# Performance work log

Measured on AMD Instinct MI355X. Metric: run time of the kernel, lower is better.

Reference implementation:

```python
import jax, jax.numpy as jnp
import numpy as np

# ---- static config (mirrors init_kwargs) ----
B, N, C_IN, C_OUT = 4, 8192, 128, 256
RATIO = 0.25
M = int(N * RATIO)          # sampled centers per cloud (fps ratio)
RADIUS = 0.1
MAX_NN = 64                 # max_num_neighbors
K = 16                      # num kernel points
D_MID = C_IN // 2           # pre_mlp: in_features -> in_features // 2
KP_EXTENT = RADIUS          # kernel-point influence extent (linear influence)


def setup_inputs() -> dict:
    key = jax.random.key(0)
    ks = jax.random.split(key, 10)
    x = jax.random.normal(ks[0], (B, N, C_IN), jnp.float32)
    pos = jax.random.uniform(ks[1], (B, N, 3), jnp.float32)  # unit cube
    W_pre = jax.random.normal(ks[2], (C_IN, D_MID), jnp.float32) / np.sqrt(C_IN).astype(np.float32)
    b_pre = jnp.zeros((D_MID,), jnp.float32)
    kp_pos = jax.random.normal(ks[3], (K, 3), jnp.float32) * (0.3 * RADIUS)
    kp_W = jax.random.normal(ks[4], (K, D_MID, D_MID), jnp.float32) / np.sqrt(D_MID * K).astype(np.float32)
    W_post = jax.random.normal(ks[5], (D_MID, C_OUT), jnp.float32) / np.sqrt(D_MID).astype(np.float32)
    b_post = jnp.zeros((C_OUT,), jnp.float32)
    W_sc = jax.random.normal(ks[6], (C_IN, C_OUT), jnp.float32) / np.sqrt(C_IN).astype(np.float32)
    b_sc = jnp.zeros((C_OUT,), jnp.float32)
    return dict(x=x, pos=pos, W_pre=W_pre, b_pre=b_pre, kp_pos=kp_pos, kp_W=kp_W,
                W_post=W_post, b_post=b_post, W_sc=W_sc, b_sc=b_sc)


def _fps(p):
    """Farthest point sampling on one cloud p:[N,3] -> idx:[M] (start at point 0)."""
    mind = jnp.sum((p - p[0]) ** 2, axis=-1)  # [N]
    def step(mind, _):
        i = jnp.argmax(mind).astype(jnp.int32)
        mind = jnp.minimum(mind, jnp.sum((p - p[i]) ** 2, axis=-1))
        return mind, i
    _, rest = jax.lax.scan(step, mind, None, length=M - 1)
    return jnp.concatenate([jnp.zeros((1,), jnp.int32), rest])


def reference(x, pos, W_pre, b_pre, kp_pos, kp_W, W_post, b_post, W_sc, b_sc):
    def _cloud(xb, pb):
        # xb:[N,C_IN], pb:[N,3]
        idx = _fps(pb)                                   # [M]
        centers = pb[idx]                                # [M,3]
        # radius neighbor search: nearest MAX_NN, mask to ball of RADIUS
        d2 = jnp.sum((centers[:, None, :] - pb[None, :, :]) ** 2, axis=-1)   # [M,N]
        neg_d2, nn_idx = jax.lax.top_k(-d2, MAX_NN)      # [M,MAX_NN]
        valid = (-neg_d2) <= RADIUS ** 2                 # [M,MAX_NN]
        # pre mlp then gather neighbor features (x_j)
        x_pre = xb @ W_pre + b_pre                       # [N,D_MID]
        x_j = x_pre[nn_idx]                              # [M,MAX_NN,D_MID]
        # kernel-point conv: linear influence of each kernel point
        rel = pb[nn_idx] - centers[:, None, :]           # [M,MAX_NN,3]
        dist = jnp.sqrt(jnp.sum((rel[:, :, None, :] - kp_pos[None, None, :, :]) ** 2, axis=-1) + 1e-12)  # [M,MAX_NN,K]
        infl = jnp.maximum(1.0 - dist / KP_EXTENT, 0.0) * valid[:, :, None]
        # aggregate (sum over neighbors) per kernel point, then contract with kernel weights
        s = jnp.einsum('mek,med->mkd', infl, x_j)        # [M,K,D_MID]
        feat = jnp.einsum('mkd,kdo->mo', s, kp_W)        # [M,D_MID]
        feat = feat @ W_post + b_post                    # [M,C_OUT]
        short = xb[idx] @ W_sc + b_sc                    # residual shortcut on sampled points
        return feat + short, centers

    out_feat, out_pos = jax.vmap(_cloud)(x, pos)         # [B,M,C_OUT], [B,M,3]
    return out_feat, out_pos
```

## Files before the change

### kernel.cpp

```cpp
#include <hip/hip_runtime.h>

#define B_    4
#define N_    8192
#define CIN   128
#define COUT  256
#define M_    2048
#define K_    16
#define DM    64
#define MAXNN 64
#define CAP   128
#define R2    0.01f
#define EXT   0.1f

#define NPRE  1024
#define CONV0 (4 + NPRE)
#define PUB   32

#define FLG(i) ((i) * 32)
#define PREFLG 128

typedef float v2f __attribute__((ext_vector_type(2)));
typedef unsigned long long ull;

__device__ __forceinline__ float d2_exact(float ax, float ay, float az,
                                          float bx, float by, float bz) {
    float dx = ax - bx, dy = ay - by, dz = az - bz;
    return __fadd_rn(__fadd_rn(__fmul_rn(dx, dx), __fmul_rn(dy, dy)), __fmul_rn(dz, dz));
}

#define DPP_STEP2(CTRL)                                                                   \
    {                                                                                     \
        unsigned tlo = (unsigned)__builtin_amdgcn_update_dpp(0, (int)klo, CTRL, 0xF, 0xF, true); \
        unsigned thi = (unsigned)__builtin_amdgcn_update_dpp(0, (int)khi, CTRL, 0xF, 0xF, true); \
        unsigned long long tk = ((unsigned long long)thi << 32) | tlo;                    \
        unsigned long long ck = ((unsigned long long)khi << 32) | klo;                    \
        if (tk > ck) { klo = tlo; khi = thi; }                                            \
    }

__global__ void init_kernel(int* __restrict__ flags) {
    if (threadIdx.x < 160) flags[threadIdx.x] = 0;
}

__global__ __launch_bounds__(512, 2) void mega_kernel(const float* __restrict__ pos,
                                                      int* __restrict__ idx_out,
                                                      float* __restrict__ out_pos,
                                                      const float* __restrict__ x,
                                                      const float* __restrict__ Wp,
                                                      const float* __restrict__ bvec,
                                                      float* __restrict__ xpre,
                                                      const float* __restrict__ kp_pos,
                                                      const float* __restrict__ kp_W,
                                                      const float* __restrict__ W_post,
                                                      const float* __restrict__ b_post,
                                                      const float* __restrict__ W_sc,
                                                      const float* __restrict__ b_sc,
                                                      float* __restrict__ out_feat,
                                                      int* __restrict__ flags) {
    __shared__ union {
        struct { float sx[N_]; float sy[N_]; float sz[N_]; ull slots[2][8]; } f;
        struct { float Ws[CIN * DM]; float xs[32][CIN]; } p;
        struct { int nIdx[CAP]; float nD2[CAP]; int cntS;
                 float infl[MAXNN][K_]; float xj[MAXNN][DM];
                 float sS[K_ * DM]; float featP[4][DM]; float xg[CIN]; } c;
    } sh;

    const int t = threadIdx.x;
    const int blk = blockIdx.x;

    if (blk >= CONV0) {
        const int cid = blk - CONV0;
        const int cb = cid & 3;
        const int cm = cid >> 2;

        if (t == 0) {
            for (;;) {
                int cur = __hip_atomic_load(&flags[FLG(cb)], __ATOMIC_RELAXED, __HIP_MEMORY_SCOPE_AGENT);
                int pre = __hip_atomic_load(&flags[PREFLG], __ATOMIC_RELAXED, __HIP_MEMORY_SCOPE_AGENT);
                if (cur > cm && pre >= NPRE) break;
                int dist = cm - cur;
                if (dist > 512)      __builtin_amdgcn_s_sleep(127);
                else if (dist > 64)  __builtin_amdgcn_s_sleep(32);
                else                 __builtin_amdgcn_s_sleep(8);
            }
            __threadfence();
            sh.c.cntS = 0;
        }
        __syncthreads();

        const float* pb = pos + (size_t)cb * N_ * 3;
        const int ctr = idx_out[cb * M_ + cm];
        const float ccx = pb[ctr * 3 + 0], ccy = pb[ctr * 3 + 1], ccz = pb[ctr * 3 + 2];

        for (int j = 0; j < N_ / 512; j++) {
            int n = j * 512 + t;
            float x0 = pb[n * 3 + 0], y0 = pb[n * 3 + 1], z0 = pb[n * 3 + 2];
            float d = d2_exact(x0, y0, z0, ccx, ccy, ccz);
            if (d <= R2) {
                int pp = atomicAdd(&sh.c.cntS, 1);
                if (pp < CAP) { sh.c.nIdx[pp] = n; sh.c.nD2[pp] = d; }
            }
        }
        __syncthreads();
        int cnt = sh.c.cntS; if (cnt > CAP) cnt = CAP;
        if (cnt > MAXNN) {
            if (t == 0) {
                for (int s = 0; s < MAXNN; s++) {
                    int best = s;
                    for (int q = s + 1; q < cnt; q++) {
                        if (sh.c.nD2[q] < sh.c.nD2[best] ||
                            (sh.c.nD2[q] == sh.c.nD2[best] && sh.c.nIdx[q] < sh.c.nIdx[best])) best = q;
                    }
                    float td = sh.c.nD2[best]; sh.c.nD2[best] = sh.c.nD2[s]; sh.c.nD2[s] = td;
                    int ti = sh.c.nIdx[best]; sh.c.nIdx[best] = sh.c.nIdx[s]; sh.c.nIdx[s] = ti;
                }
            }
            __syncthreads();
            cnt = MAXNN;
        }

        if (t < cnt) {
            int n = sh.c.nIdx[t];
            float rx = pb[n * 3 + 0] - ccx, ry = pb[n * 3 + 1] - ccy, rz = pb[n * 3 + 2] - ccz;
#pragma unroll
            for (int k = 0; k < K_; k++) {
                float dx = rx - kp_pos[k * 3 + 0];
                float dy = ry - kp_pos[k * 3 + 1];
                float dz = rz - kp_pos[k * 3 + 2];
                float dist = sqrtf(dx * dx + dy * dy + dz * dz + 1e-12f);
                sh.c.infl[t][k] = fmaxf(1.0f - dist / EXT, 0.0f);
            }
        }
        for (int i = t; i < cnt * DM; i += 512) {
            int e = i >> 6, d = i & 63;
            sh.c.xj[e][d] = xpre[((size_t)cb * N_ + sh.c.nIdx[e]) * DM + d];
        }
        __syncthreads();

        if (t < 256) {
#pragma unroll
            for (int p4 = 0; p4 < 4; p4++) {
                int pair = t + p4 * 256;
                int k = pair >> 6, d = pair & 63;
                float acc = 0.f;
                for (int e = 0; e < cnt; e++) acc = fmaf(sh.c.infl[e][k], sh.c.xj[e][d], acc);
                sh.c.sS[pair] = acc;
            }
        }
        __syncthreads();

        if (t < 256) {
            int dprime = t & 63, ks = t >> 6;
            float acc = 0.f;
            for (int k = ks * 4; k < ks * 4 + 4; k++) {
                const float* kw = kp_W + ((size_t)k * DM) * DM + dprime;
#pragma unroll
                for (int d = 0; d < DM; d++) acc = fmaf(sh.c.sS[k * DM + d], kw[d * DM], acc);
            }
            sh.c.featP[ks][dprime] = acc;
        }
        __syncthreads();
        if (t < DM) sh.c.featP[0][t] = sh.c.featP[0][t] + sh.c.featP[1][t] + sh.c.featP[2][t] + sh.c.featP[3][t];
        if (t < CIN) sh.c.xg[t] = x[((size_t)cb * N_ + ctr) * CIN + t];
        __syncthreads();

        if (t < 256) {
            const int o = t;
            float acc = b_post[o] + b_sc[o];
#pragma unroll 8
            for (int d = 0; d < DM; d++) acc = fmaf(sh.c.featP[0][d], W_post[d * COUT + o], acc);
#pragma unroll 8
            for (int cc = 0; cc < CIN; cc++) acc = fmaf(sh.c.xg[cc], W_sc[cc * COUT + o], acc);
            out_feat[((size_t)(cb * M_ + cm)) * COUT + o] = acc;
        }
        return;
    }

    if (blk >= 4) {
        const size_t rowBase = (size_t)(blk - 4) * 32;
        for (int i = t; i < CIN * DM; i += 512) sh.p.Ws[i] = Wp[i];
        for (int i = t; i < 32 * CIN; i += 512) {
            int r = i >> 7, c = i & 127;
            sh.p.xs[r][c] = x[(rowBase + r) * CIN + c];
        }
        __syncthreads();
        const int col = t & 63, r0 = t >> 6;
        float acc[4];
        float bias = bvec[col];
#pragma unroll
        for (int rr = 0; rr < 4; rr++) acc[rr] = bias;
        for (int c = 0; c < CIN; c++) {
            float w = sh.p.Ws[c * DM + col];
#pragma unroll
            for (int rr = 0; rr < 4; rr++) acc[rr] = fmaf(sh.p.xs[r0 + 8 * rr][c], w, acc[rr]);
        }
#pragma unroll
        for (int rr = 0; rr < 4; rr++) xpre[(rowBase + r0 + 8 * rr) * DM + col] = acc[rr];
        __threadfence();
        __syncthreads();
        if (t == 0) atomicAdd(&flags[PREFLG], 1);
        return;
    }

    const int b = blk;
    const float* pb = pos + (size_t)b * N_ * 3;

    v2f px[8], py[8], pz[8], mind[8];
#pragma unroll
    for (int jj = 0; jj < 8; jj++) {
        int n0 = t + (2 * jj) * 512, n1 = n0 + 512;
        float x0 = pb[n0 * 3 + 0], y0 = pb[n0 * 3 + 1], z0 = pb[n0 * 3 + 2];
        float x1 = pb[n1 * 3 + 0], y1 = pb[n1 * 3 + 1], z1 = pb[n1 * 3 + 2];
        px[jj] = (v2f){x0, x1};
        py[jj] = (v2f){y0, y1};
        pz[jj] = (v2f){z0, z1};
        mind[jj] = (v2f){1e30f, 1e30f};
        sh.f.sx[n0] = x0; sh.f.sy[n0] = y0; sh.f.sz[n0] = z0;
        sh.f.sx[n1] = x1; sh.f.sy[n1] = y1; sh.f.sz[n1] = z1;
    }
    float cx = pb[0], cy = pb[1], cz = pb[2];
    if (t == 0) {
        idx_out[b * M_ + 0] = 0;
        float* op = out_pos + ((size_t)(b * M_ + 0)) * 3;
        op[0] = cx; op[1] = cy; op[2] = cz;
    }
    __syncthreads();

    for (int m = 1; m < M_; m++) {
        float bv = -1.0f; int bj = 0;
        {
#pragma clang fp contract(off)
            v2f cx2 = (v2f){cx, cx}, cy2 = (v2f){cy, cy}, cz2 = (v2f){cz, cz};
#pragma unroll
            for (int jj = 0; jj < 8; jj++) {
                v2f dx = px[jj] - cx2, dy = py[jj] - cy2, dz = pz[jj] - cz2;
                v2f d = (dx * dx + dy * dy) + dz * dz;
                v2f mo = mind[jj];
                float n0 = fminf(mo.x, d.x);
                float n1 = fminf(mo.y, d.y);
                mind[jj] = (v2f){n0, n1};
                if (n0 > bv) { bv = n0; bj = 2 * jj; }
                if (n1 > bv) { bv = n1; bj = 2 * jj + 1; }
            }
        }
        const int bn = t + (bj << 9);
        unsigned klo = ~(unsigned)bn;
        unsigned khi = __float_as_uint(bv);

        DPP_STEP2(0x111)
        DPP_STEP2(0x112)
        DPP_STEP2(0x114)
        DPP_STEP2(0x118)
        DPP_STEP2(0x142)
        DPP_STEP2(0x143)

        ull* sl = sh.f.slots[m & 1];
        if ((t & 63) == 63) sl[t >> 6] = ((ull)khi << 32) | klo;
        __syncthreads();

        ull k0 = sl[0], k1 = sl[1], k2 = sl[2], k3 = sl[3];
        ull k4 = sl[4], k5 = sl[5], k6 = sl[6], k7 = sl[7];
        ull a0 = k0 > k1 ? k0 : k1;
        ull a1 = k2 > k3 ? k2 : k3;
        ull a2 = k4 > k5 ? k4 : k5;
        ull a3 = k6 > k7 ? k6 : k7;
        ull b0 = a0 > a1 ? a0 : a1;
        ull b1 = a2 > a3 ? a2 : a3;
        ull kk = b0 > b1 ? b0 : b1;

        const unsigned widx = ~(unsigned)(kk & 0xFFFFFFFFull);
        cx = sh.f.sx[widx]; cy = sh.f.sy[widx]; cz = sh.f.sz[widx];
        if (t == 0) {
            idx_out[b * M_ + m] = (int)widx;
            float* op = out_pos + ((size_t)(b * M_ + m)) * 3;
            op[0] = cx; op[1] = cy; op[2] = cz;
            if ((m & (PUB - 1)) == (PUB - 1)) {
                __threadfence();
                __hip_atomic_store(&flags[FLG(b)], m + 1, __ATOMIC_RELAXED, __HIP_MEMORY_SCOPE_AGENT);
            }
        }
    }
}

extern "C" void kernel_launch(void* const* d_in, const int* in_sizes, int n_in,
                              void* d_out, int out_size, void* d_ws, size_t ws_size,
                              hipStream_t stream) {
    const float* x      = (const float*)d_in[0];
    const float* pos    = (const float*)d_in[1];
    const float* W_pre  = (const float*)d_in[2];
    const float* b_pre  = (const float*)d_in[3];
    const float* kp_pos = (const float*)d_in[4];
    const float* kp_W   = (const float*)d_in[5];
    const float* W_post = (const float*)d_in[6];
    const float* b_post = (const float*)d_in[7];
    const float* W_sc   = (const float*)d_in[8];
    const float* b_sc   = (const float*)d_in[9];

    float* out_feat = (float*)d_out;
    float* out_pos  = (float*)d_out + (size_t)B_ * M_ * COUT;

    int*   idxs  = (int*)d_ws;
    int*   flags = (int*)((char*)d_ws + 48 * 1024);
    float* xpre  = (float*)((char*)d_ws + 64 * 1024);

    init_kernel<<<1, 256, 0, stream>>>(flags);
    mega_kernel<<<CONV0 + B_ * M_, 512, 0, stream>>>(pos, idxs, out_pos,
                                                     x, W_pre, b_pre, xpre,
                                                     kp_pos, kp_W, W_post, b_post,
                                                     W_sc, b_sc, out_feat, flags);
}
```

Baseline: 1.946 ms.

## Pack two FPS clouds per block and fetch winners from global memory

The farthest-point-sampling stage now runs two clouds per 512-thread block, 256 threads each holding 32 points in registers. This halves the number of FPS blocks and removes the shared-memory position copy. The winning center is now read from global (cached) memory instead of LDS, and the conv-block spin-wait is simplified to a fixed sleep. The trade-off is twice the per-thread work per FPS step, a block-wide barrier shared by both clouds, and a global-load latency on the serial FPS critical path.

```diff
diff --git a/kernel.cpp b/kernel.cpp
--- a/kernel.cpp
+++ b/kernel.cpp
@@ -13,7 +13,7 @@
 #define EXT   0.1f
 
 #define NPRE  1024
-#define CONV0 (4 + NPRE)
+#define CONV0 (2 + NPRE)
 #define PUB   32
 
 #define FLG(i) ((i) * 32)
@@ -57,7 +57,7 @@
                                                       float* __restrict__ out_feat,
                                                       int* __restrict__ flags) {
     __shared__ union {
-        struct { float sx[N_]; float sy[N_]; float sz[N_]; ull slots[2][8]; } f;
+        struct { ull slots[2][2][4]; } f;
         struct { float Ws[CIN * DM]; float xs[32][CIN]; } p;
         struct { int nIdx[CAP]; float nD2[CAP]; int cntS;
                  float infl[MAXNN][K_]; float xj[MAXNN][DM];
@@ -73,14 +73,9 @@
         const int cm = cid >> 2;
 
         if (t == 0) {
-            for (;;) {
-                int cur = __hip_atomic_load(&flags[FLG(cb)], __ATOMIC_RELAXED, __HIP_MEMORY_SCOPE_AGENT);
-                int pre = __hip_atomic_load(&flags[PREFLG], __ATOMIC_RELAXED, __HIP_MEMORY_SCOPE_AGENT);
-                if (cur > cm && pre >= NPRE) break;
-                int dist = cm - cur;
-                if (dist > 512)      __builtin_amdgcn_s_sleep(127);
-                else if (dist > 64)  __builtin_amdgcn_s_sleep(32);
-                else                 __builtin_amdgcn_s_sleep(8);
+            while (__hip_atomic_load(&flags[FLG(cb)], __ATOMIC_RELAXED, __HIP_MEMORY_SCOPE_AGENT) <= cm ||
+                   __hip_atomic_load(&flags[PREFLG], __ATOMIC_RELAXED, __HIP_MEMORY_SCOPE_AGENT) < NPRE) {
+                __builtin_amdgcn_s_sleep(64);
             }
             __threadfence();
             sh.c.cntS = 0;
@@ -175,8 +170,8 @@
         return;
     }
 
-    if (blk >= 4) {
-        const size_t rowBase = (size_t)(blk - 4) * 32;
+    if (blk >= 2) {
+        const size_t rowBase = (size_t)(blk - 2) * 32;
         for (int i = t; i < CIN * DM; i += 512) sh.p.Ws[i] = Wp[i];
         for (int i = t; i < 32 * CIN; i += 512) {
             int r = i >> 7, c = i & 127;
@@ -201,24 +196,22 @@
         return;
     }
 
-    const int b = blk;
+    const int cg = t >> 8;
+    const int lt = t & 255;
+    const int b = 2 * blk + cg;
     const float* pb = pos + (size_t)b * N_ * 3;
 
-    v2f px[8], py[8], pz[8], mind[8];
-#pragma unroll
-    for (int jj = 0; jj < 8; jj++) {
-        int n0 = t + (2 * jj) * 512, n1 = n0 + 512;
-        float x0 = pb[n0 * 3 + 0], y0 = pb[n0 * 3 + 1], z0 = pb[n0 * 3 + 2];
-        float x1 = pb[n1 * 3 + 0], y1 = pb[n1 * 3 + 1], z1 = pb[n1 * 3 + 2];
-        px[jj] = (v2f){x0, x1};
-        py[jj] = (v2f){y0, y1};
-        pz[jj] = (v2f){z0, z1};
+    v2f px[16], py[16], pz[16], mind[16];
+#pragma unroll
+    for (int jj = 0; jj < 16; jj++) {
+        int n0 = lt + (2 * jj) * 256, n1 = n0 + 256;
+        px[jj] = (v2f){pb[n0 * 3 + 0], pb[n1 * 3 + 0]};
+        py[jj] = (v2f){pb[n0 * 3 + 1], pb[n1 * 3 + 1]};
+        pz[jj] = (v2f){pb[n0 * 3 + 2], pb[n1 * 3 + 2]};
         mind[jj] = (v2f){1e30f, 1e30f};
-        sh.f.sx[n0] = x0; sh.f.sy[n0] = y0; sh.f.sz[n0] = z0;
-        sh.f.sx[n1] = x1; sh.f.sy[n1] = y1; sh.f.sz[n1] = z1;
     }
     float cx = pb[0], cy = pb[1], cz = pb[2];
-    if (t == 0) {
+    if (lt == 0) {
         idx_out[b * M_ + 0] = 0;
         float* op = out_pos + ((size_t)(b * M_ + 0)) * 3;
         op[0] = cx; op[1] = cy; op[2] = cz;
@@ -231,7 +224,7 @@
 #pragma clang fp contract(off)
             v2f cx2 = (v2f){cx, cx}, cy2 = (v2f){cy, cy}, cz2 = (v2f){cz, cz};
 #pragma unroll
-            for (int jj = 0; jj < 8; jj++) {
+            for (int jj = 0; jj < 16; jj++) {
                 v2f dx = px[jj] - cx2, dy = py[jj] - cy2, dz = pz[jj] - cz2;
                 v2f d = (dx * dx + dy * dy) + dz * dz;
                 v2f mo = mind[jj];
@@ -242,7 +235,7 @@
                 if (n1 > bv) { bv = n1; bj = 2 * jj + 1; }
             }
         }
-        const int bn = t + (bj << 9);
+        const int bn = lt + (bj << 8);
         unsigned klo = ~(unsigned)bn;
         unsigned khi = __float_as_uint(bv);
 
@@ -253,23 +246,19 @@
         DPP_STEP2(0x142)
         DPP_STEP2(0x143)
 
-        ull* sl = sh.f.slots[m & 1];
-        if ((t & 63) == 63) sl[t >> 6] = ((ull)khi << 32) | klo;
+        ull* sl = sh.f.slots[cg][m & 1];
+        if ((t & 63) == 63) sl[(t >> 6) & 3] = ((ull)khi << 32) | klo;
         __syncthreads();
 
         ull k0 = sl[0], k1 = sl[1], k2 = sl[2], k3 = sl[3];
-        ull k4 = sl[4], k5 = sl[5], k6 = sl[6], k7 = sl[7];
         ull a0 = k0 > k1 ? k0 : k1;
         ull a1 = k2 > k3 ? k2 : k3;
-        ull a2 = k4 > k5 ? k4 : k5;
-        ull a3 = k6 > k7 ? k6 : k7;
-        ull b0 = a0 > a1 ? a0 : a1;
-        ull b1 = a2 > a3 ? a2 : a3;
-        ull kk = b0 > b1 ? b0 : b1;
+        ull kk = a0 > a1 ? a0 : a1;
 
         const unsigned widx = ~(unsigned)(kk & 0xFFFFFFFFull);
-        cx = sh.f.sx[widx]; cy = sh.f.sy[widx]; cz = sh.f.sz[widx];
-        if (t == 0) {
+        const float* cp = pb + (size_t)widx * 3;
+        cx = cp[0]; cy = cp[1]; cz = cp[2];
+        if (lt == 0) {
             idx_out[b * M_ + m] = (int)widx;
             float* op = out_pos + ((size_t)(b * M_ + m)) * 3;
             op[0] = cx; op[1] = cy; op[2] = cz;
```

After: 3.523 ms. 81.0% more time.
